# Kernel optimization log

Measured on AMD Instinct MI355X. Metric: run time of the kernel, lower is better.

The kernel has to match this reference:

```python
import jax, jax.numpy as jnp
import numpy as np

EPS = 1e-5

def _ln(t, g, b):
    m = t.mean(-1, keepdims=True)
    v = ((t - m) ** 2).mean(-1, keepdims=True)
    return (t - m) * jax.lax.rsqrt(v + EPS) * g + b

def _sr(t, w, b, H, W, sr):
    # t: [B, H*W, C] -> spatial-reduction conv -> [B, (H//sr)*(W//sr), C]
    B, L, C = t.shape
    xi = t.transpose(0, 2, 1).reshape(B, C, H, W)
    y = jax.lax.conv_general_dilated(xi, w, (sr, sr), 'VALID',
                                     dimension_numbers=('NCHW', 'OIHW', 'NCHW'))
    return y.reshape(B, C, -1).transpose(0, 2, 1) + b

def setup_inputs() -> dict:
    key = jax.random.key(0)
    ks = jax.random.split(key, 9)
    C, head, sr, H, W = 128, 2, 2, 64, 64
    B, N = 4, 2 * H * W
    s = 0.02
    return {
        'x': jax.random.normal(ks[0], (B, N, C), jnp.float32),
        'qW': jax.random.normal(ks[1], (C, C), jnp.float32) * s,
        'qb': jnp.zeros((C,), jnp.float32),
        'kvW': jax.random.normal(ks[2], (C, 2 * C), jnp.float32) * s,
        'kvb': jnp.zeros((2 * C,), jnp.float32),
        'projW': jax.random.normal(ks[3], (C, C), jnp.float32) * s,
        'projb': jnp.zeros((C,), jnp.float32),
        'srW': jax.random.normal(ks[4], (C, C, sr, sr), jnp.float32) * s,
        'srb': jnp.zeros((C,), jnp.float32),
        'lnW': jnp.ones((C,), jnp.float32),
        'lnB': jnp.zeros((C,), jnp.float32),
        'H': H, 'W': W, 'fuse': 1,
    }

def reference(x, qW, qb, kvW, kvb, projW, projb, srW, srb, lnW, lnB, H, W, fuse):
    head, sr = 2, 2
    B, N, C = x.shape
    Dh = C // head
    scale = Dh ** -0.5
    q = (x @ qW + qb).reshape(B, N, head, Dh).transpose(0, 2, 1, 3)  # [B,h,N,Dh]
    mask = None
    if fuse and sr > 1:
        half = N // 2
        x_rgb = _ln(_sr(x[:, :half, :], srW, srb, H, W, sr), lnW, lnB)
        x_dte = _ln(_sr(x[:, half:, :], srW, srb, H, W, sr), lnW, lnB)
        xkv = jnp.concatenate([x_rgb, x_dte], axis=1)
        M = N // (sr * sr)
        row = jnp.arange(N)[:, None] < half            # query in rgb half
        col = jnp.arange(M)[None, :] < (M // 2)        # key in rgb half
        mask = row == col                              # True on same-modality blocks -> masked
    elif sr > 1:
        xkv = _ln(_sr(x, srW, srb, H, W, sr), lnW, lnB)
    else:
        xkv = x
    M = xkv.shape[1]
    kv = (xkv @ kvW + kvb).reshape(B, M, 2, head, Dh).transpose(2, 0, 3, 1, 4)
    k, v = kv[0], kv[1]                                # [B,h,M,Dh]
    attn = jnp.einsum('bhnd,bhmd->bhnm', q, k) * scale
    if mask is not None:
        attn = jnp.where(mask[None, None], -jnp.inf, attn)
    attn = jax.nn.softmax(attn, axis=-1)
    out = jnp.einsum('bhnm,bhmd->bhnd', attn, v).transpose(0, 2, 1, 3).reshape(B, N, C)
    return out @ projW + projb
```

## Files before the change

kernel.cpp:

```cpp
#include <hip/hip_runtime.h>
#include <hip/hip_bf16.h>

#define LN_EPS 1e-5f

typedef __attribute__((ext_vector_type(8))) short bf16x8_t;
typedef __attribute__((ext_vector_type(4))) short bf16x4_t;
typedef __attribute__((ext_vector_type(4))) float f32x4_t;
typedef __attribute__((ext_vector_type(4))) unsigned short u16x4_t;

#define MFMA32(a, b, c) __builtin_amdgcn_mfma_f32_16x16x32_bf16(a, b, c, 0, 0, 0)
#define MFMA16(a, b, c) __builtin_amdgcn_mfma_f32_16x16x16bf16_1k(a, b, c, 0, 0, 0)

__device__ inline float fast_exp2(float x) {
#if __has_builtin(__builtin_amdgcn_exp2f)
    return __builtin_amdgcn_exp2f(x);
#else
    float r;
    asm volatile("v_exp_f32 %0, %1\n\ts_nop 0" : "=v"(r) : "v"(x));
    return r;
#endif
}

__device__ inline unsigned short f2bf(float f) {
    union { float f; unsigned int u; } v; v.f = f;
    unsigned int r = v.u + 0x7fffu + ((v.u >> 16) & 1u);
    return (unsigned short)(r >> 16);
}

__device__ inline u16x4_t pk4(float a, float b, float c, float d) {
    union { u16x4_t v; __hip_bfloat162 h[2]; } u;
    u.h[0] = __float22bfloat162_rn(float2{a, b});
    u.h[1] = __float22bfloat162_rn(float2{c, d});
    return u.v;
}
__device__ inline bf16x4_t pk4b(float a, float b, float c, float d) {
    union { bf16x4_t v; __hip_bfloat162 h[2]; } u;
    u.h[0] = __float22bfloat162_rn(float2{a, b});
    u.h[1] = __float22bfloat162_rn(float2{c, d});
    return u.v;
}
__device__ inline bf16x8_t pk8(float4 a, float4 b) {
    union { bf16x8_t v; __hip_bfloat162 h[4]; } u;
    u.h[0] = __float22bfloat162_rn(float2{a.x, a.y});
    u.h[1] = __float22bfloat162_rn(float2{a.z, a.w});
    u.h[2] = __float22bfloat162_rn(float2{b.x, b.y});
    u.h[3] = __float22bfloat162_rn(float2{b.z, b.w});
    return u.v;
}

__device__ inline size_t fragidx(int row, int k, int KC) {
    return ((size_t)((row >> 4) * KC + (k >> 5))) * 512 +
           (((k >> 3) & 3) * 16 + (row & 15)) * 8 + (k & 7);
}

__global__ void k_prep_w(const float* __restrict__ qW, const float* __restrict__ kvW,
                         const float* __restrict__ projW, const float* __restrict__ srW,
                         unsigned short* __restrict__ qWs, unsigned short* __restrict__ kvWs,
                         unsigned short* __restrict__ projWs, unsigned short* __restrict__ srWs) {
    int i = blockIdx.x * 256 + threadIdx.x;
    if (i < 16384) {
        int n = i & 127, k = i >> 7;
        qWs[fragidx(n, k, 4)] = f2bf(qW[k * 128 + n]);
    } else if (i < 49152) {
        int j = i - 16384; int n = j & 255, k = j >> 8;
        kvWs[fragidx(n, k, 4)] = f2bf(kvW[k * 256 + n]);
    } else if (i < 65536) {
        int j = i - 49152; int n = j & 127, k = j >> 7;
        projWs[fragidx(n, k, 4)] = f2bf(projW[k * 128 + n]);
    } else {
        int j = i - 65536; int n = j >> 9, rem = j & 511, q = rem >> 7, c = rem & 127;
        srWs[fragidx(n, q * 128 + c, 16)] = f2bf(srW[n * 512 + c * 4 + q]);
    }
}

__global__ __launch_bounds__(256)
void k_convkv(const float* __restrict__ x, const unsigned short* __restrict__ srWs,
              const float* __restrict__ srb, const float* __restrict__ lnW,
              const float* __restrict__ lnB, const unsigned short* __restrict__ kvWs,
              const float* __restrict__ kvb, unsigned short* __restrict__ ksw,
              unsigned short* __restrict__ vls) {
    const int t = threadIdx.x, w = t >> 6, lane = t & 63;
    const int col = lane & 15, quad = lane >> 4;
    const int RT = blockIdx.x;

    __shared__ unsigned short xs[4 * 512];
    __shared__ float lnred[4][16][2];

    const int pos = RT * 16 + col;
    const int pb = pos >> 11, phf = (pos >> 10) & 1;
    const int poy = (pos >> 5) & 31, pox = pos & 31;
    int rowbase[4];
    #pragma unroll
    for (int q = 0; q < 4; q++) {
        int ky = q >> 1, kx = q & 1;
        int n = phf * 4096 + (2 * poy + ky) * 64 + 2 * pox + kx;
        rowbase[q] = (pb * 8192 + n) * 128;
    }

    f32x4_t acc[2] = {};
    {
        const unsigned short* wp = srWs + lane * 8;
        #pragma unroll
        for (int kc = 0; kc < 16; kc++) {
            const float* xr = x + rowbase[kc >> 2] + (kc & 3) * 32 + quad * 8;
            float4 xa = *(const float4*)(xr);
            float4 xb2 = *(const float4*)(xr + 4);
            bf16x8_t xb = pk8(xa, xb2);
            #pragma unroll
            for (int jj = 0; jj < 2; jj++) {
                bf16x8_t wf = *(const bf16x8_t*)(wp + (size_t)((w * 2 + jj) * 16 + kc) * 512);
                acc[jj] = MFMA32(wf, xb, acc[jj]);
            }
        }
    }
    float s = 0.f, ss = 0.f;
    #pragma unroll
    for (int jj = 0; jj < 2; jj++) {
        float4 bs = *(const float4*)(srb + (w * 2 + jj) * 16 + quad * 4);
        acc[jj][0] += bs.x; acc[jj][1] += bs.y; acc[jj][2] += bs.z; acc[jj][3] += bs.w;
        #pragma unroll
        for (int r = 0; r < 4; r++) { float v = acc[jj][r]; s += v; ss += v * v; }
    }
    s += __shfl_xor(s, 16, 64);  s += __shfl_xor(s, 32, 64);
    ss += __shfl_xor(ss, 16, 64); ss += __shfl_xor(ss, 32, 64);
    if (lane < 16) { lnred[w][lane][0] = s; lnred[w][lane][1] = ss; }
    __syncthreads();
    float stot = 0.f, sstot = 0.f;
    #pragma unroll
    for (int ww = 0; ww < 4; ww++) { stot += lnred[ww][col][0]; sstot += lnred[ww][col][1]; }
    float mean = stot * (1.0f / 128.0f);
    float var = sstot * (1.0f / 128.0f) - mean * mean;
    float rs = rsqrtf(var + LN_EPS);
    #pragma unroll
    for (int jj = 0; jj < 2; jj++) {
        int f0 = (w * 2 + jj) * 16 + quad * 4;
        float4 g = *(const float4*)(lnW + f0);
        float4 be = *(const float4*)(lnB + f0);
        u16x4_t o = pk4((acc[jj][0] - mean) * rs * g.x + be.x,
                        (acc[jj][1] - mean) * rs * g.y + be.y,
                        (acc[jj][2] - mean) * rs * g.z + be.z,
                        (acc[jj][3] - mean) * rs * g.w + be.w);
        *(u16x4_t*)(xs + ((size_t)(f0 >> 5)) * 512 +
                    (((f0 >> 3) & 3) * 16 + col) * 8 + (f0 & 7)) = o;
    }
    __syncthreads();
    bf16x8_t xf[4];
    #pragma unroll
    for (int kc = 0; kc < 4; kc++)
        xf[kc] = *(const bf16x8_t*)(xs + (size_t)kc * 512 + lane * 8);
    const int p0 = RT * 16;
    const int bb = p0 >> 11;
    #pragma unroll
    for (int jj = 0; jj < 2; jj++) {
        const int nt = w * 2 + jj;
        f32x4_t aK = {};
        #pragma unroll
        for (int kc = 0; kc < 4; kc++) {
            bf16x8_t wf = *(const bf16x8_t*)(kvWs + (size_t)(nt * 4 + kc) * 512 + lane * 8);
            aK = MFMA32(wf, xf[kc], aK);
        }
        float4 bs = *(const float4*)(kvb + nt * 16 + quad * 4);
        int m = (p0 + col) & 2047;
        int bh = bb * 2 + (nt >> 2);
        int d0 = (nt & 3) * 16 + quad * 4;
        u16x4_t o = pk4(aK[0] + bs.x, aK[1] + bs.y, aK[2] + bs.z, aK[3] + bs.w);
        *(u16x4_t*)(ksw + ((size_t)(bh * 128 + (m >> 4)) * 2 + (d0 >> 5)) * 512 +
                    (((d0 >> 3) & 3) * 16 + (m & 15)) * 8 + (d0 & 7)) = o;
    }
    #pragma unroll
    for (int jj = 0; jj < 2; jj++) {
        const int nt = w * 2 + jj;
        f32x4_t aV = {};
        #pragma unroll
        for (int kc = 0; kc < 4; kc++) {
            bf16x8_t wf = *(const bf16x8_t*)(kvWs + (size_t)((8 + nt) * 4 + kc) * 512 + lane * 8);
            aV = MFMA32(xf[kc], wf, aV);
        }
        int fv = nt * 16 + col;
        int h = fv >> 6, dd = fv & 63;
        float bv = kvb[128 + fv];
        int m0 = (p0 + quad * 4) & 2047;
        int bh = bb * 2 + h;
        int kt = m0 >> 6, nb = (m0 >> 4) & 3;
        u16x4_t o = pk4(aV[0] + bv, aV[1] + bv, aV[2] + bv, aV[3] + bv);
        *(u16x4_t*)(vls + (((size_t)(bh * 32 + kt) * 4 + (dd >> 4)) * 2 + (nb >> 1)) * 512 +
                    (quad * 16 + (dd & 15)) * 8 + (nb & 1) * 4) = o;
    }
}

__global__ __launch_bounds__(256)
void k_attn_f5(const float* __restrict__ x, const unsigned short* __restrict__ qWs,
               const float* __restrict__ qb, const unsigned short* __restrict__ ksw,
               const unsigned short* __restrict__ vls, const unsigned short* __restrict__ projWs,
               const float* __restrict__ projb, float* __restrict__ out) {
    const int blkx = blockIdx.x, mod = blockIdx.y, b = blockIdx.z;
    const int t = threadIdx.x, w = t >> 6, lane = t & 63;
    const int col = lane & 15, quad = lane >> 4;
    const int qg = w & 1, h = w >> 1;
    const int bh = b * 2 + h;
    const int qbase = mod * 4096 + blkx * 64 + qg * 32;

    __shared__ unsigned short sbuf[64 * 136];

    unsigned short* qarea = sbuf + w * 2048;
    const float sc = 0.125f * 1.44269504089f;
    #pragma unroll
    for (int qt = 0; qt < 2; qt++) {
        const float* xrow = x + ((size_t)b * 8192 + qbase + qt * 16 + col) * 128;
        f32x4_t acc[4] = {};
        #pragma unroll
        for (int kc = 0; kc < 4; kc++) {
            float4 xa = *(const float4*)(xrow + kc * 32 + quad * 8);
            float4 xb2 = *(const float4*)(xrow + kc * 32 + quad * 8 + 4);
            bf16x8_t xf = pk8(xa, xb2);
            #pragma unroll
            for (int j = 0; j < 4; j++) {
                bf16x8_t wf = *(const bf16x8_t*)(qWs + (size_t)((h * 4 + j) * 4 + kc) * 512 + lane * 8);
                acc[j] = MFMA32(wf, xf, acc[j]);
            }
        }
        #pragma unroll
        for (int j = 0; j < 4; j++) {
            float4 bs = *(const float4*)(qb + h * 64 + j * 16 + quad * 4);
            u16x4_t o = pk4((acc[j][0] + bs.x) * sc, (acc[j][1] + bs.y) * sc,
                            (acc[j][2] + bs.z) * sc, (acc[j][3] + bs.w) * sc);
            *(u16x4_t*)(qarea + ((size_t)(qt * 2 + (j >> 1))) * 512 +
                        (((j & 1) * 2 + (quad >> 1)) * 16 + col) * 8 + (quad & 1) * 4) = o;
        }
    }
    bf16x8_t qf[2][2];
    #pragma unroll
    for (int qt = 0; qt < 2; qt++)
        #pragma unroll
        for (int kc = 0; kc < 2; kc++)
            qf[qt][kc] = *(const bf16x8_t*)(qarea + (size_t)(qt * 2 + kc) * 512 + lane * 8);
    __syncthreads();

    const unsigned short* kp0 =
        ksw + ((size_t)(bh * 128 + (1 - mod) * 64) * 2) * 512 + lane * 8;
    const unsigned short* vp0 =
        vls + ((size_t)(bh * 32 + (1 - mod) * 16) * 8) * 512 + lane * 8;
    const bf16x4_t ones4 = { 0x3F80, 0x3F80, 0x3F80, 0x3F80 };

    f32x4_t O[2][4] = {};
    f32x4_t accl[2] = {};

    for (int kt = 0; kt < 16; kt++) {
        bf16x8_t kf[8];
        #pragma unroll
        for (int i = 0; i < 8; i++)
            kf[i] = *(const bf16x8_t*)(kp0 + (size_t)(kt * 8 + i) * 512);
        union { bf16x8_t v8; bf16x4_t v4[2]; } vf[8];
        #pragma unroll
        for (int i = 0; i < 8; i++)
            vf[i].v8 = *(const bf16x8_t*)(vp0 + (size_t)(kt * 8 + i) * 512);
        f32x4_t ST[2][4];
        #pragma unroll
        for (int qt = 0; qt < 2; qt++)
            #pragma unroll
            for (int nb = 0; nb < 4; nb++) {
                f32x4_t sA = {};
                sA = MFMA32(kf[nb * 2 + 0], qf[qt][0], sA);
                sA = MFMA32(kf[nb * 2 + 1], qf[qt][1], sA);
                ST[qt][nb] = sA;
            }
        bf16x4_t pa[2][4];
        #pragma unroll
        for (int qt = 0; qt < 2; qt++)
            #pragma unroll
            for (int nb = 0; nb < 4; nb++)
                pa[qt][nb] = pk4b(fast_exp2(ST[qt][nb][0]), fast_exp2(ST[qt][nb][1]),
                                  fast_exp2(ST[qt][nb][2]), fast_exp2(ST[qt][nb][3]));
        #pragma unroll
        for (int qt = 0; qt < 2; qt++) {
            #pragma unroll
            for (int nb = 0; nb < 4; nb++) {
                accl[qt] = MFMA16(pa[qt][nb], ones4, accl[qt]);
                #pragma unroll
                for (int dt = 0; dt < 4; dt++)
                    O[qt][dt] = MFMA16(pa[qt][nb], vf[dt * 2 + (nb >> 1)].v4[nb & 1], O[qt][dt]);
            }
        }
    }

    #pragma unroll
    for (int qt = 0; qt < 2; qt++) {
        #pragma unroll
        for (int r = 0; r < 4; r++) {
            float rl = 1.0f / accl[qt][r];
            int qrow = qg * 32 + qt * 16 + quad * 4 + r;
            #pragma unroll
            for (int dt = 0; dt < 4; dt++)
                sbuf[qrow * 136 + h * 64 + dt * 16 + col] = f2bf(O[qt][dt][r] * rl);
        }
    }
    __syncthreads();
    {
        const int qt2 = w;
        bf16x8_t ob[4];
        #pragma unroll
        for (int kc = 0; kc < 4; kc++)
            ob[kc] = *(const bf16x8_t*)(sbuf + (size_t)(qt2 * 16 + col) * 136 + kc * 32 + quad * 8);
        f32x4_t acc[8];
        #pragma unroll
        for (int j = 0; j < 8; j++) acc[j] = f32x4_t{};
        #pragma unroll
        for (int kc = 0; kc < 4; kc++)
            #pragma unroll
            for (int j = 0; j < 8; j++) {
                bf16x8_t wf = *(const bf16x8_t*)(projWs + (size_t)(j * 4 + kc) * 512 + lane * 8);
                acc[j] = MFMA32(wf, ob[kc], acc[j]);
            }
        const int n = b * 8192 + mod * 4096 + blkx * 64 + qt2 * 16 + col;
        #pragma unroll
        for (int j = 0; j < 8; j++) {
            int f0 = j * 16 + quad * 4;
            float4 bs = *(const float4*)(projb + f0);
            float4 o = { acc[j][0] + bs.x, acc[j][1] + bs.y,
                         acc[j][2] + bs.z, acc[j][3] + bs.w };
            *(float4*)(out + (size_t)n * 128 + f0) = o;
        }
    }
}

extern "C" void kernel_launch(void* const* d_in, const int* in_sizes, int n_in,
                              void* d_out, int out_size, void* d_ws, size_t ws_size,
                              hipStream_t stream) {
    const float* x     = (const float*)d_in[0];
    const float* qW    = (const float*)d_in[1];
    const float* qb    = (const float*)d_in[2];
    const float* kvW   = (const float*)d_in[3];
    const float* kvb   = (const float*)d_in[4];
    const float* projW = (const float*)d_in[5];
    const float* projb = (const float*)d_in[6];
    const float* srW   = (const float*)d_in[7];
    const float* srb   = (const float*)d_in[8];
    const float* lnW   = (const float*)d_in[9];
    const float* lnB   = (const float*)d_in[10];

    char* ws = (char*)d_ws;
    unsigned short* qWs    = (unsigned short*)(ws + 0);
    unsigned short* kvWs   = (unsigned short*)(ws + 32768);
    unsigned short* projWs = (unsigned short*)(ws + 98304);
    unsigned short* srWs   = (unsigned short*)(ws + 131072);
    unsigned short* ksw    = (unsigned short*)(ws + 262144);
    unsigned short* vls    = (unsigned short*)(ws + 2359296);

    k_prep_w<<<dim3(512), dim3(256), 0, stream>>>(qW, kvW, projW, srW,
                                                  qWs, kvWs, projWs, srWs);
    k_convkv<<<dim3(512), dim3(256), 0, stream>>>(x, srWs, srb, lnW, lnB,
                                                  kvWs, kvb, ksw, vls);
    k_attn_f5<<<dim3(64, 2, 4), dim3(256), 0, stream>>>(x, qWs, qb, ksw, vls,
                                                        projWs, projb, (float*)d_out);
}
```

Baseline: 136.9 us.

## Stage conv input in LDS and double-buffer K/V fragment loads in attention

```diff
diff --git a/kernel.cpp b/kernel.cpp
--- a/kernel.cpp
+++ b/kernel.cpp
@@ -73,6 +73,7 @@
     }
 }
 
+#define XPAD 132
 __global__ __launch_bounds__(256)
 void k_convkv(const float* __restrict__ x, const unsigned short* __restrict__ srWs,
               const float* __restrict__ srb, const float* __restrict__ lnW,
@@ -83,29 +84,32 @@
     const int col = lane & 15, quad = lane >> 4;
     const int RT = blockIdx.x;
 
+    __shared__ unsigned short xl[64 * XPAD];
     __shared__ unsigned short xs[4 * 512];
     __shared__ float lnred[4][16][2];
 
-    const int pos = RT * 16 + col;
-    const int pb = pos >> 11, phf = (pos >> 10) & 1;
-    const int poy = (pos >> 5) & 31, pox = pos & 31;
-    int rowbase[4];
-    #pragma unroll
-    for (int q = 0; q < 4; q++) {
-        int ky = q >> 1, kx = q & 1;
-        int n = phf * 4096 + (2 * poy + ky) * 64 + 2 * pox + kx;
-        rowbase[q] = (pb * 8192 + n) * 128;
-    }
+    const int pb = RT >> 7, phf = (RT >> 6) & 1;
+    const int oy = (RT >> 1) & 31, ox0 = (RT & 1) * 16;
+    const int n0 = phf * 4096 + 2 * oy * 64 + 2 * ox0;
+    #pragma unroll
+    for (int it = 0; it < 8; it++) {
+        int idx = it * 256 + t;
+        int chunk = idx >> 10;
+        int rr = (idx >> 5) & 31;
+        int c4 = idx & 31;
+        float4 v = *(const float4*)(x + ((size_t)(pb * 8192 + n0 + chunk * 64 + rr)) * 128 + c4 * 4);
+        *(u16x4_t*)(xl + (chunk * 32 + rr) * XPAD + c4 * 4) = pk4(v.x, v.y, v.z, v.w);
+    }
+    __syncthreads();
 
     f32x4_t acc[2] = {};
     {
         const unsigned short* wp = srWs + lane * 8;
         #pragma unroll
         for (int kc = 0; kc < 16; kc++) {
-            const float* xr = x + rowbase[kc >> 2] + (kc & 3) * 32 + quad * 8;
-            float4 xa = *(const float4*)(xr);
-            float4 xb2 = *(const float4*)(xr + 4);
-            bf16x8_t xb = pk8(xa, xb2);
+            const int q = kc >> 2, cg = kc & 3;
+            const int r = (q >> 1) * 32 + 2 * col + (q & 1);
+            bf16x8_t xb = *(const bf16x8_t*)(xl + r * XPAD + cg * 32 + quad * 8);
             #pragma unroll
             for (int jj = 0; jj < 2; jj++) {
                 bf16x8_t wf = *(const bf16x8_t*)(wp + (size_t)((w * 2 + jj) * 16 + kc) * 512);
@@ -188,8 +192,8 @@
     }
 }
 
-__global__ __launch_bounds__(256)
-void k_attn_f5(const float* __restrict__ x, const unsigned short* __restrict__ qWs,
+__global__ __launch_bounds__(256, 2)
+void k_attn_f6(const float* __restrict__ x, const unsigned short* __restrict__ qWs,
                const float* __restrict__ qb, const unsigned short* __restrict__ ksw,
                const unsigned short* __restrict__ vls, const unsigned short* __restrict__ projWs,
                const float* __restrict__ projb, float* __restrict__ out) {
@@ -245,23 +249,33 @@
     f32x4_t O[2][4] = {};
     f32x4_t accl[2] = {};
 
-    for (int kt = 0; kt < 16; kt++) {
-        bf16x8_t kf[8];
-        #pragma unroll
-        for (int i = 0; i < 8; i++)
-            kf[i] = *(const bf16x8_t*)(kp0 + (size_t)(kt * 8 + i) * 512);
-        union { bf16x8_t v8; bf16x4_t v4[2]; } vf[8];
-        #pragma unroll
-        for (int i = 0; i < 8; i++)
-            vf[i].v8 = *(const bf16x8_t*)(vp0 + (size_t)(kt * 8 + i) * 512);
+    union vun { bf16x8_t v8; bf16x4_t v4[2]; };
+    bf16x8_t kf0[8], kf1[8];
+    vun vf0[8], vf1[8];
+
+    auto pref0 = [&](int kt) {
+        #pragma unroll
+        for (int i = 0; i < 8; i++) {
+            kf0[i] = *(const bf16x8_t*)(kp0 + (size_t)(kt * 8 + i) * 512);
+            vf0[i].v8 = *(const bf16x8_t*)(vp0 + (size_t)(kt * 8 + i) * 512);
+        }
+    };
+    auto pref1 = [&](int kt) {
+        #pragma unroll
+        for (int i = 0; i < 8; i++) {
+            kf1[i] = *(const bf16x8_t*)(kp0 + (size_t)(kt * 8 + i) * 512);
+            vf1[i].v8 = *(const bf16x8_t*)(vp0 + (size_t)(kt * 8 + i) * 512);
+        }
+    };
+    auto body = [&](bf16x8_t (&kfc)[8], vun (&vfc)[8]) {
         f32x4_t ST[2][4];
         #pragma unroll
         for (int qt = 0; qt < 2; qt++)
             #pragma unroll
             for (int nb = 0; nb < 4; nb++) {
                 f32x4_t sA = {};
-                sA = MFMA32(kf[nb * 2 + 0], qf[qt][0], sA);
-                sA = MFMA32(kf[nb * 2 + 1], qf[qt][1], sA);
+                sA = MFMA32(kfc[nb * 2 + 0], qf[qt][0], sA);
+                sA = MFMA32(kfc[nb * 2 + 1], qf[qt][1], sA);
                 ST[qt][nb] = sA;
             }
         bf16x4_t pa[2][4];
@@ -278,9 +292,18 @@
                 accl[qt] = MFMA16(pa[qt][nb], ones4, accl[qt]);
                 #pragma unroll
                 for (int dt = 0; dt < 4; dt++)
-                    O[qt][dt] = MFMA16(pa[qt][nb], vf[dt * 2 + (nb >> 1)].v4[nb & 1], O[qt][dt]);
-            }
-        }
+                    O[qt][dt] = MFMA16(pa[qt][nb], vfc[dt * 2 + (nb >> 1)].v4[nb & 1], O[qt][dt]);
+            }
+        }
+    };
+
+    pref0(0);
+    #pragma unroll
+    for (int kt2 = 0; kt2 < 8; kt2++) {
+        pref1(kt2 * 2 + 1);
+        body(kf0, vf0);
+        if (kt2 < 7) pref0(kt2 * 2 + 2);
+        body(kf1, vf1);
     }
 
     #pragma unroll
@@ -350,6 +373,6 @@
                                                   qWs, kvWs, projWs, srWs);
     k_convkv<<<dim3(512), dim3(256), 0, stream>>>(x, srWs, srb, lnW, lnB,
                                                   kvWs, kvb, ksw, vls);
-    k_attn_f5<<<dim3(64, 2, 4), dim3(256), 0, stream>>>(x, qWs, qb, ksw, vls,
+    k_attn_f6<<<dim3(64, 2, 4), dim3(256), 0, stream>>>(x, qWs, qb, ksw, vls,
                                                         projWs, projb, (float*)d_out);
 }
```

After: 133.8 us. 2.2% less time.
